# Optimization experiments

Hardware: AMD Instinct MI355X
Metric: run time of the kernel (lower is better)

The kernel has to match this reference:

```python
import jax, jax.numpy as jnp
import numpy as np


def setup_inputs() -> dict:
    key = jax.random.key(0)
    ks = jax.random.split(key, 12)
    b, c, h, w = 2, 128, 256, 512          # x: [b,c,h,w], h == d_model
    n_cond, d_cond, d_attn = 512, 512, 256  # single head: d_attn = n_heads*d_head = 256
    return {
        "x": jax.random.normal(ks[0], (b, c, h, w), jnp.float32),
        "v": jax.random.normal(ks[1], (b, n_cond, d_cond), jnp.float32),
        "Wq": jax.random.normal(ks[2], (h, d_attn), jnp.float32) * 0.05,
        "Wk": jax.random.normal(ks[3], (d_cond, d_attn), jnp.float32) * 0.05,
        "Wv": jax.random.normal(ks[4], (d_cond, d_attn), jnp.float32) * 0.05,
        "Wo": jax.random.normal(ks[5], (d_attn, h), jnp.float32) * 0.05,
        "bo": jnp.zeros((h,), jnp.float32),
        "mask_w": jax.random.normal(ks[6], (h,), jnp.float32),  # ConvTranspose2d(1,1,(1,h)) weight, applied to ones -> just the kernel
        "conv_w": jax.random.normal(ks[7], (c, 2 * c, 3, 3), jnp.float32) * 0.02,
        "conv_b": jnp.zeros((c,), jnp.float32),
        "gn_gamma": jnp.ones((c,), jnp.float32),
        "gn_beta": jnp.zeros((c,), jnp.float32),
    }


def reference(x, v, Wq, Wk, Wv, Wo, bo, mask_w, conv_w, conv_b, gn_gamma, gn_beta):
    b, c, h, w = x.shape
    # ---- CrossAttention (note: self.scale defined but never applied in source) ----
    xt = jnp.swapaxes(x, 2, 3)                        # [b,c,w,h]
    q = jnp.einsum("bcwh,hd->bcwd", xt, Wq)           # [b,c,w,d_attn]
    k = jnp.einsum("bnd,de->bne", v, Wk)              # [b,n_cond,d_attn]
    val = jnp.einsum("bnd,de->bne", v, Wv)
    attn = jnp.einsum("bcwd,bnd->bcwn", q, k)         # [b,c,w,n_cond]
    attn = jax.nn.softmax(attn, axis=-1)
    out = jnp.einsum("bcwn,bnd->bcwd", attn, val)     # [b,c,w,d_attn]
    out = jnp.einsum("bcwd,dh->bcwh", out, Wo) + bo   # [b,c,w,h]
    attn_feature = jnp.swapaxes(out, 2, 3)            # [b,c,h,w]

    # ---- NonAdaptiveLearnedMask (eval mode: no Gaussian noise) ----
    sig = jax.nn.sigmoid(mask_w)                      # [h]
    x2 = jnp.broadcast_to(sig[None, :], (b, h))       # [b,h]
    k_keep = int(h * (1.0 - 0.2))                     # p=0.2 hardcoded in module
    topval = jax.lax.top_k(x2, k_keep)[0][:, -1:]     # kth-largest per row [b,1]
    comp = (x2 >= topval).astype(x2.dtype)
    wta = comp * x2                                   # sparsified sigmoid outputs
    slope = 1.0
    probs = jax.nn.sigmoid(slope * wta)
    hard = (probs > 0.5).astype(x2.dtype)             # straight-through binary act
    binary = probs + jax.lax.stop_gradient(hard - probs)  # [b,h]
    binary_mask = jnp.broadcast_to(binary[:, None, None, :], (b, 1, w, h))
    masked_x = jnp.swapaxes(binary_mask * jnp.swapaxes(x, 2, 3), 2, 3)  # [b,c,h,w]

    # ---- conv3x3 on concat + GroupNorm + SiLU ----
    cat = jnp.concatenate([masked_x, attn_feature], axis=1)  # [b,2c,h,w]
    hh = jax.lax.conv_general_dilated(
        cat, conv_w, window_strides=(1, 1), padding="SAME",
        dimension_numbers=("NCHW", "OIHW", "NCHW"))
    hh = hh + conv_b[None, :, None, None]
    g = min(c // 4, 32)
    hr = hh.reshape(b, g, c // g, h, w)
    mean = hr.mean(axis=(2, 3, 4), keepdims=True)
    var = hr.var(axis=(2, 3, 4), keepdims=True)
    hn = ((hr - mean) * jax.lax.rsqrt(var + 1e-6)).reshape(b, c, h, w)
    hn = hn * gn_gamma[None, :, None, None] + gn_beta[None, :, None, None]
    out = hn * jax.nn.sigmoid(hn)  # SiLU
    return (out, binary_mask)
```

## Files before the change

### kernel.cpp

```cpp
#include <hip/hip_runtime.h>
#include <math.h>

#define B      2
#define C      128
#define H      256
#define W      512
#define NCOND  512
#define DCOND  512
#define DATTN  256
#define KKEEP  204

#define WS_CATN   0ull
#define WS_KQ     134742016ull
#define WS_VOT    135266304ull
#define WS_W9     135790592ull
#define WS_BIN    136380416ull
#define WS_ST2    136381440ull

typedef __attribute__((ext_vector_type(8))) short bf16x8;
typedef __attribute__((ext_vector_type(4))) float f32x4;

union U8 { bf16x8 v; ushort u[8]; };

__device__ inline ushort f2bf(float f) {
    union { float f; unsigned u; } v; v.f = f;
    unsigned r = v.u + 0x7fffu + ((v.u >> 16) & 1u);
    return (ushort)(r >> 16);
}

__device__ __forceinline__ void gld16(const ushort* g, void* l) {
    __builtin_amdgcn_global_load_lds(
        (const __attribute__((address_space(1))) unsigned int*)(const void*)g,
        (__attribute__((address_space(3))) unsigned int*)l, 16, 0, 0);
}

__global__ void k_binary(const float* __restrict__ mask_w, float* __restrict__ bin) {
    __shared__ float s[H];
    int t = threadIdx.x;
    float sv = 1.0f / (1.0f + __expf(-mask_w[t]));
    s[t] = sv;
    __syncthreads();
    int cnt = 0;
    for (int j = 0; j < H; ++j) cnt += (s[j] > sv) ? 1 : 0;
    bin[t] = (cnt < KKEEP) ? 1.0f : 0.0f;
}

__global__ void k_maskout(const float* __restrict__ bin, float* __restrict__ mout) {
    int i = blockIdx.x * 256 + threadIdx.x;
    if (i < B * W * H) mout[i] = bin[i & (H - 1)];
}

__launch_bounds__(256)
__global__ void k_kv(const float* __restrict__ v, const float* __restrict__ Wk,
                     const float* __restrict__ Wv, const float* __restrict__ Wq,
                     const float* __restrict__ Wo, ushort* __restrict__ kqc,
                     ushort* __restrict__ voc) {
    __shared__ float vrow[DCOND];
    __shared__ float kld[DATTN];
    __shared__ float vld[DATTN];
    int bn = blockIdx.x;
    int t  = threadIdx.x;
    const float* vp = v + (size_t)bn * DCOND;
    for (int i = t; i < DCOND; i += 256) vrow[i] = vp[i];
    __syncthreads();
    float ka = 0.f, va = 0.f;
    for (int d4 = 0; d4 < DCOND / 4; ++d4) {
        float4 vv = *(const float4*)(vrow + d4 * 4);
        const float* wk = Wk + (d4 * 4) * DATTN + t;
        const float* wv = Wv + (d4 * 4) * DATTN + t;
        ka += vv.x * wk[0];         va += vv.x * wv[0];
        ka += vv.y * wk[DATTN];     va += vv.y * wv[DATTN];
        ka += vv.z * wk[2 * DATTN]; va += vv.z * wv[2 * DATTN];
        ka += vv.w * wk[3 * DATTN]; va += vv.w * wv[3 * DATTN];
    }
    kld[t] = ka; vld[t] = va;
    __syncthreads();
    float kq = 0.f;
    const float4* wqr = (const float4*)(Wq + (size_t)t * DATTN);
#pragma unroll 8
    for (int d4 = 0; d4 < DATTN / 4; ++d4) {
        float4 w = wqr[d4];
        kq += kld[d4 * 4] * w.x + kld[d4 * 4 + 1] * w.y
            + kld[d4 * 4 + 2] * w.z + kld[d4 * 4 + 3] * w.w;
    }
    float vo = 0.f;
#pragma unroll 8
    for (int d = 0; d < DATTN; ++d) vo += vld[d] * Wo[(size_t)d * 256 + t];

    int b = bn >> 9, n = bn & 511;
    {
        int s    = ((t >> 6) << 1) | (n >> 8);
        int nl   = n & 255;
        int slot = (((t >> 3) & 7) ^ (n & 7));
        kqc[(((size_t)(b * 8 + s)) * 256 + nl) * 64 + slot * 8 + (t & 7)] = f2bf(kq);
    }
    {
        int s2   = n >> 6;
        int slot = (((n >> 3) & 7) ^ (t & 7));
        voc[(((size_t)(b * 8 + s2)) * 256 + t) * 64 + slot * 8 + (n & 7)] = f2bf(vo);
    }
}

__global__ void k_w9p(const float* __restrict__ cw, ushort* __restrict__ w9p) {
    int i = blockIdx.x * 256 + threadIdx.x;
    if (i >= 294912) return;
    int cp = i >> 13;
    int r  = i & 8191;
    int co = r >> 6;
    int u  = r & 63;
    int us = u >> 3, j = u & 7;
    int c  = cp / 9, p = cp - c * 9;
    int cc = ((us ^ (co & 7)) << 3) | j;
    int ci = c * 64 + cc;
    w9p[(size_t)cp * 8192 + co * 64 + u] = f2bf(cw[(co * 256 + ci) * 9 + p]);
}

__launch_bounds__(256)
__global__ void k_attn(const float* __restrict__ x, const ushort* __restrict__ kqc,
                       const ushort* __restrict__ voc, const float* __restrict__ bo,
                       ushort* __restrict__ af16) {
    __shared__ __align__(16) char arena[33792];
    __shared__ __align__(16) char bbuf[32768];
    float* smax = (float*)(arena + 32768);
    float* ssum = (float*)(arena + 33280);

    const int t   = threadIdx.x;
    const int ln  = t & 63;
    const int blk = blockIdx.x;
    const int b   = blk >> 11;
    const int ci  = (blk >> 4) & 127;
    const int w0  = (blk & 15) << 5;
    const int wid = t >> 6;
    const int lr  = t & 15;
    const int lg  = (t & 63) >> 4;

    {
        const float* xp = x + (((size_t)b * C + ci) * H + t) * W + w0;
#pragma unroll
        for (int j4 = 0; j4 < 8; ++j4) {
            float4 v4 = *(const float4*)(xp + j4 * 4);
            int j = j4 * 4;
            *(ushort*)(arena + (j + 0) * 512 + ((2 * t) ^ (((j + 0) & 7) << 4))) = f2bf(v4.x);
            *(ushort*)(arena + (j + 1) * 512 + ((2 * t) ^ (((j + 1) & 7) << 4))) = f2bf(v4.y);
            *(ushort*)(arena + (j + 2) * 512 + ((2 * t) ^ (((j + 2) & 7) << 4))) = f2bf(v4.z);
            *(ushort*)(arena + (j + 3) * 512 + ((2 * t) ^ (((j + 3) & 7) << 4))) = f2bf(v4.w);
        }
    }

    float rinv[2][4];
    {
        f32x4 sac[2][8];
#pragma unroll
        for (int mb = 0; mb < 2; ++mb)
#pragma unroll
            for (int g = 0; g < 8; ++g) sac[mb][g] = (f32x4){0.f, 0.f, 0.f, 0.f};
        const ushort* kqb = kqc + (size_t)b * 131072;
        for (int s = 0; s < 8; ++s) {
            __syncthreads();
            const ushort* src = kqb + s * 16384;
#pragma unroll
            for (int i = 0; i < 8; ++i) {
                int q = wid * 8 + i;
                gld16(src + q * 512 + ln * 8, bbuf + q * 1024);
            }
            __syncthreads();
#pragma unroll
            for (int ksl = 0; ksl < 2; ++ksl) {
                int gks = (s >> 1) * 2 + ksl;
                int kb = (gks * 64 + lg * 16) ^ ((lr & 7) << 4);
                bf16x8 a0 = *(const bf16x8*)(arena + lr * 512 + kb);
                bf16x8 a1 = *(const bf16x8*)(arena + (16 + lr) * 512 + kb);
#pragma unroll
                for (int nb = 0; nb < 4; ++nb) {
                    int nl = wid * 64 + nb * 16 + lr;
                    int slot = (ksl * 4 + lg) ^ (nl & 7);
                    bf16x8 bf = *(const bf16x8*)(bbuf + nl * 128 + slot * 16);
                    int g = (s & 1) * 4 + nb;
                    sac[0][g] = __builtin_amdgcn_mfma_f32_16x16x32_bf16(a0, bf, sac[0][g], 0, 0, 0);
                    sac[1][g] = __builtin_amdgcn_mfma_f32_16x16x32_bf16(a1, bf, sac[1][g], 0, 0, 0);
                }
            }
        }
        float pmax[2][4];
#pragma unroll
        for (int mb = 0; mb < 2; ++mb)
#pragma unroll
            for (int r = 0; r < 4; ++r) {
                float m = sac[mb][0][r];
#pragma unroll
                for (int g = 1; g < 8; ++g) m = fmaxf(m, sac[mb][g][r]);
#pragma unroll
                for (int o = 8; o >= 1; o >>= 1) m = fmaxf(m, __shfl_xor(m, o));
                pmax[mb][r] = m;
            }
        if (lr == 0) {
#pragma unroll
            for (int mb = 0; mb < 2; ++mb)
#pragma unroll
                for (int r = 0; r < 4; ++r)
                    smax[(mb * 16 + lg * 4 + r) * 4 + wid] = pmax[mb][r];
        }
        __syncthreads();
        float psum[2][4];
#pragma unroll
        for (int mb = 0; mb < 2; ++mb)
#pragma unroll
            for (int r = 0; r < 4; ++r) {
                int m = mb * 16 + lg * 4 + r;
                float g2 = fmaxf(fmaxf(smax[m * 4], smax[m * 4 + 1]),
                                 fmaxf(smax[m * 4 + 2], smax[m * 4 + 3]));
                float s = 0.f;
#pragma unroll
                for (int g = 0; g < 8; ++g) {
                    float e = __expf(sac[mb][g][r] - g2);
                    s += e;
                    int n = (g >> 2) * 256 + wid * 64 + (g & 3) * 16 + lr;
                    *(ushort*)(arena + m * 1024 + ((2 * n) ^ ((m & 7) << 4))) = f2bf(e);
                }
#pragma unroll
                for (int o = 8; o >= 1; o >>= 1) s += __shfl_xor(s, o);
                psum[mb][r] = s;
            }
        if (lr == 0) {
#pragma unroll
            for (int mb = 0; mb < 2; ++mb)
#pragma unroll
                for (int r = 0; r < 4; ++r)
                    ssum[(mb * 16 + lg * 4 + r) * 4 + wid] = psum[mb][r];
        }
        __syncthreads();
#pragma unroll
        for (int mb = 0; mb < 2; ++mb)
#pragma unroll
            for (int r = 0; r < 4; ++r) {
                int m = mb * 16 + lg * 4 + r;
                rinv[mb][r] = 1.0f / (ssum[m * 4] + ssum[m * 4 + 1] + ssum[m * 4 + 2] + ssum[m * 4 + 3]);
            }
    }

    {
        f32x4 oac[2][4];
#pragma unroll
        for (int mb = 0; mb < 2; ++mb)
#pragma unroll
            for (int nb = 0; nb < 4; ++nb) oac[mb][nb] = (f32x4){0.f, 0.f, 0.f, 0.f};
        const ushort* vob = voc + (size_t)b * 131072;
        for (int s2 = 0; s2 < 8; ++s2) {
            __syncthreads();
            const ushort* src = vob + s2 * 16384;
#pragma unroll
            for (int i = 0; i < 8; ++i) {
                int q = wid * 8 + i;
                gld16(src + q * 512 + ln * 8, bbuf + q * 1024);
            }
            __syncthreads();
#pragma unroll
            for (int ksl = 0; ksl < 2; ++ksl) {
                int gks = s2 * 2 + ksl;
                int kb = (gks * 64 + lg * 16) ^ ((lr & 7) << 4);
                bf16x8 a0 = *(const bf16x8*)(arena + lr * 1024 + kb);
                bf16x8 a1 = *(const bf16x8*)(arena + (16 + lr) * 1024 + kb);
#pragma unroll
                for (int nb = 0; nb < 4; ++nb) {
                    int d = wid * 64 + nb * 16 + lr;
                    int slot = (ksl * 4 + lg) ^ (d & 7);
                    bf16x8 bf = *(const bf16x8*)(bbuf + d * 128 + slot * 16);
                    oac[0][nb] = __builtin_amdgcn_mfma_f32_16x16x32_bf16(a0, bf, oac[0][nb], 0, 0, 0);
                    oac[1][nb] = __builtin_amdgcn_mfma_f32_16x16x32_bf16(a1, bf, oac[1][nb], 0, 0, 0);
                }
            }
        }
        size_t afbase = ((size_t)b * C + ci) * H * W;
#pragma unroll
        for (int nb = 0; nb < 4; ++nb) {
            int h = wid * 64 + nb * 16 + lr;
            float bias = bo[h];
            ushort* op = af16 + afbase + (size_t)h * W + w0;
#pragma unroll
            for (int mb = 0; mb < 2; ++mb) {
                ushort4 u;
                u.x = f2bf(oac[mb][nb][0] * rinv[mb][0] + bias);
                u.y = f2bf(oac[mb][nb][1] * rinv[mb][1] + bias);
                u.z = f2bf(oac[mb][nb][2] * rinv[mb][2] + bias);
                u.w = f2bf(oac[mb][nb][3] * rinv[mb][3] + bias);
                *(ushort4*)(op + mb * 16 + lg * 4) = u;
            }
        }
    }
}

__launch_bounds__(256)
__global__ void k_cat(const float* __restrict__ x, const ushort* __restrict__ af16,
                      const float* __restrict__ bin, ushort* __restrict__ catn) {
    __shared__ __align__(16) char st[32768];
    const int t   = threadIdx.x;
    const int blk = blockIdx.x;
    const int xt  = blk & 7;
    const int y   = (blk >> 3) & 255;
    const int b   = blk >> 11;
    const int x0  = xt * 64;
    const float bw = bin[y];

    for (int i = t; i < 2048; i += 256) {
        int cc = i >> 4, c4 = i & 15;
        float4 v = *(const float4*)(x + (((size_t)b * C + cc) * H + y) * W + x0 + c4 * 4);
#pragma unroll
        for (int j = 0; j < 4; ++j) {
            int px = c4 * 4 + j;
            float f = (j == 0 ? v.x : j == 1 ? v.y : j == 2 ? v.z : v.w) * bw;
            *(ushort*)(st + px * 512 + ((2 * cc) ^ ((px & 7) << 4))) = f2bf(f);
        }
    }
    for (int i = t; i < 1024; i += 256) {
        int cc = i >> 3, c8 = i & 7;
        U8 v;
        v.v = *(const bf16x8*)(af16 + (((size_t)b * C + cc) * H + y) * W + x0 + c8 * 8);
#pragma unroll
        for (int j = 0; j < 8; ++j) {
            int px = c8 * 8 + j;
            *(ushort*)(st + px * 512 + ((2 * (128 + cc)) ^ ((px & 7) << 4))) = v.u[j];
        }
    }
    __syncthreads();
    const size_t rowb = ((size_t)b * H + y) * 514;
    for (int i = t; i < 2048; i += 256) {
        int px = i >> 5, c16 = i & 31;
        int c = c16 >> 3, cgs = c16 & 7;
        int ix = x0 + px + 1;
        int cgl = cgs ^ (ix & 7);
        bf16x8 v = *(const bf16x8*)(st + px * 512 + ((((c << 3) | cgl) << 4) ^ ((px & 7) << 4)));
        *(bf16x8*)(catn + (rowb + ix) * 256 + c * 64 + cgs * 8) = v;
    }
    const bf16x8 z = {0, 0, 0, 0, 0, 0, 0, 0};
    if (xt == 0 && t < 32) *(bf16x8*)(catn + (rowb + 0) * 256 + t * 8) = z;
    if (xt == 7 && t < 32) *(bf16x8*)(catn + (rowb + 513) * 256 + t * 8) = z;
}

__launch_bounds__(512, 4)
__global__ void k_convg(const ushort* __restrict__ catn, const ushort* __restrict__ w9p,
                        const float* __restrict__ conv_b, float* __restrict__ out,
                        float* __restrict__ pb) {
    __shared__ __align__(16) char stf[55296];
    __shared__ __align__(16) char wls[16384];
    __shared__ float pst[4][64];
    const int t   = threadIdx.x;
    const int ln  = t & 63;
    const int blk = blockIdx.x;
    const int xt  = blk & 7;
    const int yq  = (blk >> 3) & 63;
    const int b   = blk >> 9;
    const int x0  = xt * 64;
    const int y0  = yq * 4;
    const int wid = t >> 6;
    const int wm  = wid >> 1;
    const int wn  = wid & 1;
    const int lr  = t & 15;
    const int lg  = (t & 63) >> 4;
    const ushort* cbase = catn + (size_t)b * ((size_t)H * 514 * 256);

    f32x4 acc[4][4];
#pragma unroll
    for (int mb = 0; mb < 4; ++mb)
#pragma unroll
        for (int nb = 0; nb < 4; ++nb) acc[mb][nb] = (f32x4){0.f, 0.f, 0.f, 0.f};

    for (int c = 0; c < 4; ++c) {
        __syncthreads();
        for (int q = wid; q < 54; q += 8) {
            int r = q / 9, seg = q - r * 9;
            int iy = y0 - 1 + r;
            char* ldsb = stf + r * 9216 + seg * 1024;
            if ((unsigned)iy < (unsigned)H) {
                const ushort* src = cbase + ((size_t)iy * 514 + x0 + seg * 8 + (ln >> 3)) * 256
                                  + c * 64 + (ln & 7) * 8;
                gld16(src, ldsb);
            } else {
                *(f32x4*)(ldsb + ln * 16) = (f32x4){0.f, 0.f, 0.f, 0.f};
            }
        }
        {
            const ushort* wsrc = w9p + (size_t)(c * 9 + 0) * 8192;
#pragma unroll
            for (int q = wid * 2; q < wid * 2 + 2; ++q)
                gld16(wsrc + q * 512 + ln * 8, wls + q * 1024);
        }
        __syncthreads();

        for (int p = 0; p < 9; ++p) {
            const int dy = p / 3, dx = p - dy * 3;
            const char* arow = stf + (wm + dy) * 9216;
#pragma unroll
            for (int ks = 0; ks < 2; ++ks) {
                bf16x8 afr[4];
#pragma unroll
                for (int mb = 0; mb < 4; ++mb) {
                    int px = mb * 16 + lr + dx;
                    afr[mb] = *(const bf16x8*)(arow + px * 128 + ((ks * 64 + lg * 16) ^ ((px & 7) << 4)));
                }
                bf16x8 bfr[4];
#pragma unroll
                for (int nb = 0; nb < 4; ++nb) {
                    int co = wn * 64 + nb * 16 + lr;
                    bfr[nb] = *(const bf16x8*)(wls + co * 128 + ((ks * 64 + lg * 16) ^ ((co & 7) << 4)));
                }
#pragma unroll
                for (int nb = 0; nb < 4; ++nb)
#pragma unroll
                    for (int mb = 0; mb < 4; ++mb)
                        acc[mb][nb] = __builtin_amdgcn_mfma_f32_16x16x32_bf16(afr[mb], bfr[nb], acc[mb][nb], 0, 0, 0);
            }
            if (p < 8) {
                __syncthreads();
                const ushort* wsrc = w9p + (size_t)(c * 9 + p + 1) * 8192;
#pragma unroll
                for (int q = wid * 2; q < wid * 2 + 2; ++q)
                    gld16(wsrc + q * 512 + ln * 8, wls + q * 1024);
                __syncthreads();
            }
        }
    }

#pragma unroll
    for (int nb = 0; nb < 4; ++nb) {
        int co = wn * 64 + nb * 16 + lr;
        float bias = conv_b[co];
        float s = 0.f, ss = 0.f;
        float* op = out + (((size_t)b * C + co) * H + (y0 + wm)) * W + x0;
#pragma unroll
        for (int mb = 0; mb < 4; ++mb) {
            float4 o = make_float4(acc[mb][nb][0] + bias, acc[mb][nb][1] + bias,
                                   acc[mb][nb][2] + bias, acc[mb][nb][3] + bias);
            s  += (o.x + o.y) + (o.z + o.w);
            ss += (o.x * o.x + o.y * o.y) + (o.z * o.z + o.w * o.w);
            *(float4*)(op + mb * 16 + lg * 4) = o;
        }
        s += __shfl_xor(s, 1);  ss += __shfl_xor(ss, 1);
        s += __shfl_xor(s, 2);  ss += __shfl_xor(ss, 2);
        s += __shfl_xor(s, 16); ss += __shfl_xor(ss, 16);
        s += __shfl_xor(s, 32); ss += __shfl_xor(ss, 32);
        if (lg == 0 && (lr & 3) == 0) {
            int g = co >> 2;
            pst[wm][g * 2]     = s;
            pst[wm][g * 2 + 1] = ss;
        }
    }
    __syncthreads();
    if (t < 64)
        pb[(size_t)blk * 64 + t] = pst[0][t] + pst[1][t] + pst[2][t] + pst[3][t];
}

__global__ void k_stats2(const float* __restrict__ pb, float* __restrict__ st2) {
    __shared__ float red[512];
    int blk = blockIdx.x;
    int b = blk >> 5, g = blk & 31;
    int t = threadIdx.x;
    float s = 0.f, ss = 0.f;
    for (int j = t; j < 512; j += 256) {
        const float* p = pb + ((size_t)(b * 512 + j)) * 64 + g * 2;
        s += p[0]; ss += p[1];
    }
    red[t * 2] = s; red[t * 2 + 1] = ss;
    __syncthreads();
    for (int o = 128; o >= 1; o >>= 1) {
        if (t < o) {
            red[t * 2]     += red[(t + o) * 2];
            red[t * 2 + 1] += red[(t + o) * 2 + 1];
        }
        __syncthreads();
    }
    if (t == 0) {
        const float inv = 1.0f / 524288.0f;
        float mean = red[0] * inv;
        float var  = red[1] * inv - mean * mean;
        st2[blk * 2]     = mean;
        st2[blk * 2 + 1] = rsqrtf(var + 1e-6f);
    }
}

__global__ void k_norm(const float* __restrict__ st2, const float* __restrict__ gamma,
                       const float* __restrict__ beta, float* __restrict__ out) {
    const int N4 = B * C * H * W / 4;
    int stride = gridDim.x * 256;
    for (int i4 = blockIdx.x * 256 + threadIdx.x; i4 < N4; i4 += stride) {
        int i = i4 * 4;
        int c = (i >> 17) & 127;
        int b = i >> 24;
        int g = c >> 2;
        float mean = st2[(b * 32 + g) * 2];
        float rstd = st2[(b * 32 + g) * 2 + 1];
        float ga = gamma[c], be = beta[c];
        float4 v = *(float4*)(out + i);
        float n0 = (v.x - mean) * rstd * ga + be;
        float n1 = (v.y - mean) * rstd * ga + be;
        float n2 = (v.z - mean) * rstd * ga + be;
        float n3 = (v.w - mean) * rstd * ga + be;
        v.x = n0 / (1.0f + __expf(-n0));
        v.y = n1 / (1.0f + __expf(-n1));
        v.z = n2 / (1.0f + __expf(-n2));
        v.w = n3 / (1.0f + __expf(-n3));
        *(float4*)(out + i) = v;
    }
}

extern "C" void kernel_launch(void* const* d_in, const int* in_sizes, int n_in,
                              void* d_out, int out_size, void* d_ws, size_t ws_size,
                              hipStream_t stream) {
    const float* x      = (const float*)d_in[0];
    const float* v      = (const float*)d_in[1];
    const float* Wq     = (const float*)d_in[2];
    const float* Wk     = (const float*)d_in[3];
    const float* Wv     = (const float*)d_in[4];
    const float* Wo     = (const float*)d_in[5];
    const float* bo     = (const float*)d_in[6];
    const float* mask_w = (const float*)d_in[7];
    const float* conv_w = (const float*)d_in[8];
    const float* conv_b = (const float*)d_in[9];
    const float* gng    = (const float*)d_in[10];
    const float* gnb    = (const float*)d_in[11];

    float* out  = (float*)d_out;
    float* mout = out + B * C * H * W;
    ushort* af16 = (ushort*)d_out;

    char*  wsb  = (char*)d_ws;
    ushort* catn  = (ushort*)(wsb + WS_CATN);
    ushort* kqc   = (ushort*)(wsb + WS_KQ);
    ushort* voc   = (ushort*)(wsb + WS_VOT);
    ushort* w9p   = (ushort*)(wsb + WS_W9);
    float*  bin   = (float*)(wsb + WS_BIN);
    float*  st2   = (float*)(wsb + WS_ST2);
    float*  pb    = (float*)(wsb + WS_KQ);

    k_binary <<<1,    256, 0, stream>>>(mask_w, bin);
    k_maskout<<<1024, 256, 0, stream>>>(bin, mout);
    k_kv     <<<B * NCOND, 256, 0, stream>>>(v, Wk, Wv, Wq, Wo, kqc, voc);
    k_w9p    <<<1152, 256, 0, stream>>>(conv_w, w9p);
    k_attn   <<<4096, 256, 0, stream>>>(x, kqc, voc, bo, af16);
    k_cat    <<<4096, 256, 0, stream>>>(x, af16, bin, catn);
    k_convg  <<<1024, 512, 0, stream>>>(catn, w9p, conv_b, out, pb);
    k_stats2 <<<64,   256, 0, stream>>>(pb, st2);
    k_norm   <<<2048, 256, 0, stream>>>(st2, gng, gnb, out);
}
```

Before: 509.1 us.

## Enlarge attention tile to 64 rows with 512 threads and double-buffered K/V loads

The attention kernel now processes 64 w-positions per block with 8 waves instead of 32 with 4, so each block loads the K and V tiles from global memory half as often per row. The staging buffer for K/V is double-buffered: the next stage is issued before computing the current one, and one barrier per stage replaces two. LDS usage roughly doubles to about 132KB per block, which may limit how many blocks fit on a CU.

```diff
diff --git a/kernel.cpp b/kernel.cpp
--- a/kernel.cpp
+++ b/kernel.cpp
@@ -115,169 +115,189 @@
     w9p[(size_t)cp * 8192 + co * 64 + u] = f2bf(cw[(co * 256 + ci) * 9 + p]);
 }
 
-__launch_bounds__(256)
+__launch_bounds__(512, 2)
 __global__ void k_attn(const float* __restrict__ x, const ushort* __restrict__ kqc,
                        const ushort* __restrict__ voc, const float* __restrict__ bo,
                        ushort* __restrict__ af16) {
-    __shared__ __align__(16) char arena[33792];
-    __shared__ __align__(16) char bbuf[32768];
-    float* smax = (float*)(arena + 32768);
-    float* ssum = (float*)(arena + 33280);
+    __shared__ __align__(16) char arena[65536];
+    __shared__ __align__(16) char bbuf[65536];
+    __shared__ float smax[512];
+    __shared__ float ssum[512];
 
     const int t   = threadIdx.x;
     const int ln  = t & 63;
     const int blk = blockIdx.x;
-    const int b   = blk >> 11;
-    const int ci  = (blk >> 4) & 127;
-    const int w0  = (blk & 15) << 5;
+    const int b   = blk >> 10;
+    const int ci  = (blk >> 3) & 127;
+    const int w0  = (blk & 7) << 6;
     const int wid = t >> 6;
     const int lr  = t & 15;
     const int lg  = (t & 63) >> 4;
 
     {
-        const float* xp = x + (((size_t)b * C + ci) * H + t) * W + w0;
+        int h = t >> 1, hf = t & 1;
+        const float* xp = x + (((size_t)b * C + ci) * H + h) * W + w0 + hf * 32;
 #pragma unroll
         for (int j4 = 0; j4 < 8; ++j4) {
             float4 v4 = *(const float4*)(xp + j4 * 4);
-            int j = j4 * 4;
-            *(ushort*)(arena + (j + 0) * 512 + ((2 * t) ^ (((j + 0) & 7) << 4))) = f2bf(v4.x);
-            *(ushort*)(arena + (j + 1) * 512 + ((2 * t) ^ (((j + 1) & 7) << 4))) = f2bf(v4.y);
-            *(ushort*)(arena + (j + 2) * 512 + ((2 * t) ^ (((j + 2) & 7) << 4))) = f2bf(v4.z);
-            *(ushort*)(arena + (j + 3) * 512 + ((2 * t) ^ (((j + 3) & 7) << 4))) = f2bf(v4.w);
-        }
-    }
-
-    float rinv[2][4];
+            int wb = hf * 32 + j4 * 4;
+            *(ushort*)(arena + (wb + 0) * 512 + ((2 * h) ^ (((wb + 0) & 7) << 4))) = f2bf(v4.x);
+            *(ushort*)(arena + (wb + 1) * 512 + ((2 * h) ^ (((wb + 1) & 7) << 4))) = f2bf(v4.y);
+            *(ushort*)(arena + (wb + 2) * 512 + ((2 * h) ^ (((wb + 2) & 7) << 4))) = f2bf(v4.z);
+            *(ushort*)(arena + (wb + 3) * 512 + ((2 * h) ^ (((wb + 3) & 7) << 4))) = f2bf(v4.w);
+        }
+    }
+
+    const ushort* kqb = kqc + (size_t)b * 131072;
+#pragma unroll
+    for (int i = 0; i < 4; ++i) {
+        int q = wid * 4 + i;
+        gld16(kqb + q * 512 + ln * 8, bbuf + q * 1024);
+    }
+    __syncthreads();
+
+    float rinv[4][4];
     {
-        f32x4 sac[2][8];
-#pragma unroll
-        for (int mb = 0; mb < 2; ++mb)
-#pragma unroll
-            for (int g = 0; g < 8; ++g) sac[mb][g] = (f32x4){0.f, 0.f, 0.f, 0.f};
-        const ushort* kqb = kqc + (size_t)b * 131072;
+        f32x4 sac[4][4];
+#pragma unroll
+        for (int mb = 0; mb < 4; ++mb)
+#pragma unroll
+            for (int g = 0; g < 4; ++g) sac[mb][g] = (f32x4){0.f, 0.f, 0.f, 0.f};
         for (int s = 0; s < 8; ++s) {
+            const char* cur = bbuf + (s & 1) * 32768;
+            if (s < 7) {
+                char* nxt = bbuf + ((s + 1) & 1) * 32768;
+                const ushort* src = kqb + (s + 1) * 16384;
+#pragma unroll
+                for (int i = 0; i < 4; ++i) {
+                    int q = wid * 4 + i;
+                    gld16(src + q * 512 + ln * 8, nxt + q * 1024);
+                }
+            }
+            int hc = s >> 1, nh = s & 1;
+#pragma unroll
+            for (int ksl = 0; ksl < 2; ++ksl) {
+                int kb = ((hc * 2 + ksl) * 64 + lg * 16) ^ ((lr & 7) << 4);
+                bf16x8 a[4];
+#pragma unroll
+                for (int mb = 0; mb < 4; ++mb)
+                    a[mb] = *(const bf16x8*)(arena + (mb * 16 + lr) * 512 + kb);
+#pragma unroll
+                for (int nb = 0; nb < 2; ++nb) {
+                    int nl = wid * 32 + nb * 16 + lr;
+                    int slot = (ksl * 4 + lg) ^ (nl & 7);
+                    bf16x8 bf = *(const bf16x8*)(cur + nl * 128 + slot * 16);
+                    int g = nh * 2 + nb;
+#pragma unroll
+                    for (int mb = 0; mb < 4; ++mb)
+                        sac[mb][g] = __builtin_amdgcn_mfma_f32_16x16x32_bf16(a[mb], bf, sac[mb][g], 0, 0, 0);
+                }
+            }
             __syncthreads();
-            const ushort* src = kqb + s * 16384;
-#pragma unroll
-            for (int i = 0; i < 8; ++i) {
-                int q = wid * 8 + i;
-                gld16(src + q * 512 + ln * 8, bbuf + q * 1024);
-            }
-            __syncthreads();
-#pragma unroll
-            for (int ksl = 0; ksl < 2; ++ksl) {
-                int gks = (s >> 1) * 2 + ksl;
-                int kb = (gks * 64 + lg * 16) ^ ((lr & 7) << 4);
-                bf16x8 a0 = *(const bf16x8*)(arena + lr * 512 + kb);
-                bf16x8 a1 = *(const bf16x8*)(arena + (16 + lr) * 512 + kb);
-#pragma unroll
-                for (int nb = 0; nb < 4; ++nb) {
-                    int nl = wid * 64 + nb * 16 + lr;
-                    int slot = (ksl * 4 + lg) ^ (nl & 7);
-                    bf16x8 bf = *(const bf16x8*)(bbuf + nl * 128 + slot * 16);
-                    int g = (s & 1) * 4 + nb;
-                    sac[0][g] = __builtin_amdgcn_mfma_f32_16x16x32_bf16(a0, bf, sac[0][g], 0, 0, 0);
-                    sac[1][g] = __builtin_amdgcn_mfma_f32_16x16x32_bf16(a1, bf, sac[1][g], 0, 0, 0);
-                }
-            }
-        }
-        float pmax[2][4];
-#pragma unroll
-        for (int mb = 0; mb < 2; ++mb)
+        }
+        float pmax[4][4];
+#pragma unroll
+        for (int mb = 0; mb < 4; ++mb)
 #pragma unroll
             for (int r = 0; r < 4; ++r) {
                 float m = sac[mb][0][r];
 #pragma unroll
-                for (int g = 1; g < 8; ++g) m = fmaxf(m, sac[mb][g][r]);
+                for (int g = 1; g < 4; ++g) m = fmaxf(m, sac[mb][g][r]);
 #pragma unroll
                 for (int o = 8; o >= 1; o >>= 1) m = fmaxf(m, __shfl_xor(m, o));
                 pmax[mb][r] = m;
             }
         if (lr == 0) {
 #pragma unroll
-            for (int mb = 0; mb < 2; ++mb)
+            for (int mb = 0; mb < 4; ++mb)
 #pragma unroll
                 for (int r = 0; r < 4; ++r)
-                    smax[(mb * 16 + lg * 4 + r) * 4 + wid] = pmax[mb][r];
+                    smax[(mb * 16 + lg * 4 + r) * 8 + wid] = pmax[mb][r];
         }
         __syncthreads();
-        float psum[2][4];
-#pragma unroll
-        for (int mb = 0; mb < 2; ++mb)
+#pragma unroll
+        for (int mb = 0; mb < 4; ++mb)
 #pragma unroll
             for (int r = 0; r < 4; ++r) {
                 int m = mb * 16 + lg * 4 + r;
-                float g2 = fmaxf(fmaxf(smax[m * 4], smax[m * 4 + 1]),
-                                 fmaxf(smax[m * 4 + 2], smax[m * 4 + 3]));
+                const float* sm = smax + m * 8;
+                float gm = fmaxf(fmaxf(fmaxf(sm[0], sm[1]), fmaxf(sm[2], sm[3])),
+                                 fmaxf(fmaxf(sm[4], sm[5]), fmaxf(sm[6], sm[7])));
                 float s = 0.f;
 #pragma unroll
-                for (int g = 0; g < 8; ++g) {
-                    float e = __expf(sac[mb][g][r] - g2);
+                for (int g = 0; g < 4; ++g) {
+                    float e = __expf(sac[mb][g][r] - gm);
                     s += e;
-                    int n = (g >> 2) * 256 + wid * 64 + (g & 3) * 16 + lr;
+                    int n = (g >> 1) * 256 + wid * 32 + (g & 1) * 16 + lr;
                     *(ushort*)(arena + m * 1024 + ((2 * n) ^ ((m & 7) << 4))) = f2bf(e);
                 }
 #pragma unroll
                 for (int o = 8; o >= 1; o >>= 1) s += __shfl_xor(s, o);
-                psum[mb][r] = s;
-            }
-        if (lr == 0) {
-#pragma unroll
-            for (int mb = 0; mb < 2; ++mb)
-#pragma unroll
-                for (int r = 0; r < 4; ++r)
-                    ssum[(mb * 16 + lg * 4 + r) * 4 + wid] = psum[mb][r];
-        }
+                if (lr == 0) ssum[m * 8 + wid] = s;
+            }
         __syncthreads();
 #pragma unroll
-        for (int mb = 0; mb < 2; ++mb)
+        for (int mb = 0; mb < 4; ++mb)
 #pragma unroll
             for (int r = 0; r < 4; ++r) {
                 int m = mb * 16 + lg * 4 + r;
-                rinv[mb][r] = 1.0f / (ssum[m * 4] + ssum[m * 4 + 1] + ssum[m * 4 + 2] + ssum[m * 4 + 3]);
+                const float* su = ssum + m * 8;
+                rinv[mb][r] = 1.0f / (((su[0] + su[1]) + (su[2] + su[3]))
+                                    + ((su[4] + su[5]) + (su[6] + su[7])));
             }
     }
 
     {
-        f32x4 oac[2][4];
-#pragma unroll
-        for (int mb = 0; mb < 2; ++mb)
-#pragma unroll
-            for (int nb = 0; nb < 4; ++nb) oac[mb][nb] = (f32x4){0.f, 0.f, 0.f, 0.f};
         const ushort* vob = voc + (size_t)b * 131072;
+#pragma unroll
+        for (int i = 0; i < 4; ++i) {
+            int q = wid * 4 + i;
+            gld16(vob + q * 512 + ln * 8, bbuf + q * 1024);
+        }
+        __syncthreads();
+        f32x4 oac[4][2];
+#pragma unroll
+        for (int mb = 0; mb < 4; ++mb)
+#pragma unroll
+            for (int nb = 0; nb < 2; ++nb) oac[mb][nb] = (f32x4){0.f, 0.f, 0.f, 0.f};
         for (int s2 = 0; s2 < 8; ++s2) {
+            const char* cur = bbuf + (s2 & 1) * 32768;
+            if (s2 < 7) {
+                char* nxt = bbuf + ((s2 + 1) & 1) * 32768;
+                const ushort* src = vob + (s2 + 1) * 16384;
+#pragma unroll
+                for (int i = 0; i < 4; ++i) {
+                    int q = wid * 4 + i;
+                    gld16(src + q * 512 + ln * 8, nxt + q * 1024);
+                }
+            }
+#pragma unroll
+            for (int ksl = 0; ksl < 2; ++ksl) {
+                int kb = ((s2 * 2 + ksl) * 64 + lg * 16) ^ ((lr & 7) << 4);
+                bf16x8 a[4];
+#pragma unroll
+                for (int mb = 0; mb < 4; ++mb)
+                    a[mb] = *(const bf16x8*)(arena + (mb * 16 + lr) * 1024 + kb);
+#pragma unroll
+                for (int nb = 0; nb < 2; ++nb) {
+                    int d = wid * 32 + nb * 16 + lr;
+                    int slot = (ksl * 4 + lg) ^ (d & 7);
+                    bf16x8 bf = *(const bf16x8*)(cur + d * 128 + slot * 16);
+#pragma unroll
+                    for (int mb = 0; mb < 4; ++mb)
+                        oac[mb][nb] = __builtin_amdgcn_mfma_f32_16x16x32_bf16(a[mb], bf, oac[mb][nb], 0, 0, 0);
+                }
+            }
             __syncthreads();
-            const ushort* src = vob + s2 * 16384;
-#pragma unroll
-            for (int i = 0; i < 8; ++i) {
-                int q = wid * 8 + i;
-                gld16(src + q * 512 + ln * 8, bbuf + q * 1024);
-            }
-            __syncthreads();
-#pragma unroll
-            for (int ksl = 0; ksl < 2; ++ksl) {
-                int gks = s2 * 2 + ksl;
-                int kb = (gks * 64 + lg * 16) ^ ((lr & 7) << 4);
-                bf16x8 a0 = *(const bf16x8*)(arena + lr * 1024 + kb);
-                bf16x8 a1 = *(const bf16x8*)(arena + (16 + lr) * 1024 + kb);
-#pragma unroll
-                for (int nb = 0; nb < 4; ++nb) {
-                    int d = wid * 64 + nb * 16 + lr;
-                    int slot = (ksl * 4 + lg) ^ (d & 7);
-                    bf16x8 bf = *(const bf16x8*)(bbuf + d * 128 + slot * 16);
-                    oac[0][nb] = __builtin_amdgcn_mfma_f32_16x16x32_bf16(a0, bf, oac[0][nb], 0, 0, 0);
-                    oac[1][nb] = __builtin_amdgcn_mfma_f32_16x16x32_bf16(a1, bf, oac[1][nb], 0, 0, 0);
-                }
-            }
         }
         size_t afbase = ((size_t)b * C + ci) * H * W;
 #pragma unroll
-        for (int nb = 0; nb < 4; ++nb) {
-            int h = wid * 64 + nb * 16 + lr;
+        for (int nb = 0; nb < 2; ++nb) {
+            int h = wid * 32 + nb * 16 + lr;
             float bias = bo[h];
             ushort* op = af16 + afbase + (size_t)h * W + w0;
 #pragma unroll
-            for (int mb = 0; mb < 2; ++mb) {
+            for (int mb = 0; mb < 4; ++mb) {
                 ushort4 u;
                 u.x = f2bf(oac[mb][nb][0] * rinv[mb][0] + bias);
                 u.y = f2bf(oac[mb][nb][1] * rinv[mb][1] + bias);
@@ -535,7 +555,7 @@
     k_maskout<<<1024, 256, 0, stream>>>(bin, mout);
     k_kv     <<<B * NCOND, 256, 0, stream>>>(v, Wk, Wv, Wq, Wo, kqc, voc);
     k_w9p    <<<1152, 256, 0, stream>>>(conv_w, w9p);
-    k_attn   <<<4096, 256, 0, stream>>>(x, kqc, voc, bo, af16);
+    k_attn   <<<2048, 512, 0, stream>>>(x, kqc, voc, bo, af16);
     k_cat    <<<4096, 256, 0, stream>>>(x, af16, bin, catn);
     k_convg  <<<1024, 512, 0, stream>>>(catn, w9p, conv_b, out, pb);
     k_stats2 <<<64,   256, 0, stream>>>(pb, st2);
```

New measurement: 517.2 us. No clear change (+1.6%).
